# Kernel optimization log

Hardware: AMD Instinct MI355X
Metric: run time of the kernel (lower is better)

Reference implementation:

```python
import jax, jax.numpy as jnp
import numpy as np


def hadamard_matrix(n):
    # Recursive normalized Hadamard matrix of size 2^n (matches the torch code).
    H = np.array([[1.0]])
    for _ in range(n):
        H = np.block([[H, H], [H, -H]]) / np.sqrt(2.0)
    return jnp.asarray(H, dtype=jnp.float32)


def hadamard_conv(x, filt, bias, H):
    # x: (B, Cin, h, w); filt: (F, kh, kw); bias: (F, 1); H: (n, n)
    n = H.shape[0]
    F, kh, kw = filt.shape
    B, C = x.shape[0], x.shape[1]
    # zero-pad filters and data up to (n, n), then 2D Hadamard transform H A H
    kern = jnp.zeros((F, n, n), x.dtype).at[:, :kh, :kw].set(filt)
    kern_t = jnp.matmul(H, jnp.matmul(kern, H))            # (F, n, n)
    data = jnp.zeros((B, C, n, n), x.dtype).at[:, :, : x.shape[2], : x.shape[3]].set(x)
    data_t = jnp.matmul(H, jnp.matmul(data, H))            # (B, C, n, n)
    # Original: expand to (B, C, F, n, n), multiply by kern_t, inverse transform,
    # then sum over C. Since kern_t is independent of C and the transforms are
    # linear, sum over C first -- identical math, no huge intermediate.
    s = data_t.sum(axis=1)                                  # (B, n, n)
    prod = s[:, None, :, :] * kern_t[None, :, :, :]         # (B, F, n, n)
    out = jnp.matmul(H, jnp.matmul(prod, H))                # (B, F, n, n)
    return out + bias[:, 0][None, :, None, None]


def maxpool2(x):
    # 2x2 max pool, stride 2, on (B, C, H, W)
    return jax.lax.reduce_window(x, -jnp.inf, jax.lax.max, (1, 1, 2, 2), (1, 1, 2, 2), 'VALID')


def setup_inputs() -> dict:
    key = jax.random.key(0)
    ks = jax.random.split(key, 9)
    return {
        'x': jax.random.normal(ks[0], (2048, 3, 32, 32), dtype=jnp.float32),
        'filter1': jax.random.normal(ks[1], (32, 3, 3), dtype=jnp.float32),
        'bias1': jax.random.normal(ks[2], (32, 1), dtype=jnp.float32),
        'filter2': jax.random.normal(ks[3], (64, 3, 3), dtype=jnp.float32),
        'bias2': jax.random.normal(ks[4], (64, 1), dtype=jnp.float32),
        'fc1_w': jax.random.normal(ks[5], (512, 4096), dtype=jnp.float32) * 0.02,
        'fc1_b': jax.random.normal(ks[6], (512,), dtype=jnp.float32) * 0.02,
        'fc2_w': jax.random.normal(ks[7], (10, 512), dtype=jnp.float32) * 0.02,
        'fc2_b': jax.random.normal(ks[8], (10,), dtype=jnp.float32) * 0.02,
    }


def reference(x, filter1, bias1, filter2, bias2, fc1_w, fc1_b, fc2_w, fc2_b):
    H1 = hadamard_matrix(5)  # 32x32
    H2 = hadamard_matrix(4)  # 16x16
    out = hadamard_conv(x, filter1, bias1, H1)      # (B, 32, 32, 32)
    out = maxpool2(jax.nn.relu(out))                # (B, 32, 16, 16)
    out = hadamard_conv(out, filter2, bias2, H2)    # (B, 64, 16, 16)
    out = maxpool2(jax.nn.relu(out))                # (B, 64, 8, 8)
    out = out.reshape(-1, 4096)
    out = jax.nn.relu(out @ fc1_w.T + fc1_b)        # (B, 512)
    out = out @ fc2_w.T + fc2_b                     # (B, 10)
    return jax.nn.softmax(out, axis=1)
```

## Files before the change

### kernel.cpp

```cpp
#include <hip/hip_runtime.h>

#define DEVI __device__ __forceinline__

typedef __attribute__((ext_vector_type(8))) short short8x;
typedef __attribute__((ext_vector_type(4))) float float4x;

DEVI float shx(float v, int m) { return __shfl_xor(v, m, 64); }

DEVI unsigned bf16r(float v) {
  unsigned u = __float_as_uint(v);
  return (u + 0x7FFF + ((u >> 16) & 1)) >> 16;
}
DEVI void split2(float a, float b, unsigned& h, unsigned& l) {
  unsigned ra = bf16r(a), rb = bf16r(b);
  float fa = __uint_as_float(ra << 16), fb = __uint_as_float(rb << 16);
  unsigned la = bf16r(a - fa), lb = bf16r(b - fb);
  h = ra | (rb << 16);
  l = la | (lb << 16);
}

DEVI void gload16(const void* g, void* l) {
  __builtin_amdgcn_global_load_lds(
      (const __attribute__((address_space(1))) void*)g,
      (__attribute__((address_space(3))) void*)l, 16, 0, 0);
}

template <int MASK>
DEVI float lanex(float x) {
  if constexpr (MASK == 1)
    return __int_as_float(__builtin_amdgcn_update_dpp(
        0, __float_as_int(x), 0xB1, 0xF, 0xF, true));
  else if constexpr (MASK == 2)
    return __int_as_float(__builtin_amdgcn_update_dpp(
        0, __float_as_int(x), 0x4E, 0xF, 0xF, true));
  else
    return __int_as_float(__builtin_amdgcn_ds_swizzle(
        __float_as_int(x), (MASK << 10) | 0x1F));
}

__global__ __launch_bounds__(256) void k_conv(
    const float* __restrict__ x, const float* __restrict__ filt1,
    const float* __restrict__ bias1, const float* __restrict__ filt2,
    const float* __restrict__ bias2, unsigned short* __restrict__ Ah,
    unsigned short* __restrict__ Al) {
  __shared__ float sP[4 * 320];
  const int b = blockIdx.x;
  const int tid = threadIdx.x;
  const int wv = tid >> 6, t = tid & 63;

  float s0[16];
  {
    const float* xb = x + (size_t)b * 3072 + (t >> 1) * 32 + (t & 1) * 16;
#pragma unroll
    for (int q = 0; q < 4; ++q) {
      float4 a0 = *(const float4*)(xb + 4 * q);
      float4 a1 = *(const float4*)(xb + 1024 + 4 * q);
      float4 a2 = *(const float4*)(xb + 2048 + 4 * q);
      s0[4 * q + 0] = (a0.x + a1.x + a2.x) * (1.0f / 32.0f);
      s0[4 * q + 1] = (a0.y + a1.y + a2.y) * (1.0f / 32.0f);
      s0[4 * q + 2] = (a0.z + a1.z + a2.z) * (1.0f / 32.0f);
      s0[4 * q + 3] = (a0.w + a1.w + a2.w) * (1.0f / 32.0f);
    }
  }
  float s1[16], s2[16];
#pragma unroll
  for (int k = 0; k < 16; ++k) s1[k] = lanex<2>(s0[k]);
#pragma unroll
  for (int k = 0; k < 16; ++k) s2[k] = lanex<4>(s0[k]);

  float acc[8];
#pragma unroll
  for (int j = 0; j < 8; ++j) acc[j] = 0.0f;

  for (int i = 0; i < 8; ++i) {
    const int f = __builtin_amdgcn_readfirstlane(wv * 8 + i);
    const float* fp = filt1 + f * 9;
    float w[9];
#pragma unroll
    for (int k = 0; k < 9; ++k) w[k] = fp[k];
    const float bb = bias1[f];
    float c[8];
#pragma unroll
    for (int p = 0; p < 8; ++p) {
      const int ja = 2 * p, jb = ja ^ 1;
      const int ja2 = ja ^ 2, jb2 = jb ^ 2;
      float va = fmaf(w[0], s0[ja], bb);
      va = fmaf(w[1], s0[jb], va);
      va = fmaf(w[2], s0[ja2], va);
      va = fmaf(w[3], s1[ja], va);
      va = fmaf(w[4], s1[jb], va);
      va = fmaf(w[5], s1[ja2], va);
      va = fmaf(w[6], s2[ja], va);
      va = fmaf(w[7], s2[jb], va);
      va = fmaf(w[8], s2[ja2], va);
      float vb = fmaf(w[0], s0[jb], bb);
      vb = fmaf(w[1], s0[ja], vb);
      vb = fmaf(w[2], s0[jb2], vb);
      vb = fmaf(w[3], s1[jb], vb);
      vb = fmaf(w[4], s1[ja], vb);
      vb = fmaf(w[5], s1[jb2], vb);
      vb = fmaf(w[6], s2[jb], vb);
      vb = fmaf(w[7], s2[ja], vb);
      vb = fmaf(w[8], s2[jb2], vb);
      c[p] = fmaxf(fmaxf(va, vb), 0.0f);
    }
#pragma unroll
    for (int p = 0; p < 8; ++p) acc[p] += fmaxf(c[p], lanex<2>(c[p]));
  }

  if (!(t & 2)) {
    const int pb = wv * 320 + (t >> 2) * 20 + (t & 1) * 8;
    *(float4*)&sP[pb] = make_float4(acc[0], acc[1], acc[2], acc[3]);
    *(float4*)&sP[pb + 4] = make_float4(acc[4], acc[5], acc[6], acc[7]);
  }
  __syncthreads();

  const int f2s = t >> 4, rr = t & 15;
  float r0[16];
#pragma unroll
  for (int q = 0; q < 4; ++q) {
    float4 s = make_float4(0.f, 0.f, 0.f, 0.f);
#pragma unroll
    for (int w2 = 0; w2 < 4; ++w2) {
      const float4 v = *(const float4*)&sP[w2 * 320 + rr * 20 + 4 * q];
      s.x += v.x; s.y += v.y; s.z += v.z; s.w += v.w;
    }
    r0[4 * q + 0] = s.x * (1.0f / 16.0f);
    r0[4 * q + 1] = s.y * (1.0f / 16.0f);
    r0[4 * q + 2] = s.z * (1.0f / 16.0f);
    r0[4 * q + 3] = s.w * (1.0f / 16.0f);
  }
  float r1[16], r2[16];
#pragma unroll
  for (int k = 0; k < 16; ++k) r1[k] = lanex<1>(r0[k]);
#pragma unroll
  for (int k = 0; k < 16; ++k) r2[k] = lanex<2>(r0[k]);

#pragma unroll
  for (int it = 0; it < 4; ++it) {
    const int g = wv * 16 + it * 4 + f2s;
    const float* gp = filt2 + g * 9;
    float w[9];
#pragma unroll
    for (int k = 0; k < 9; ++k) w[k] = gp[k];
    const float bb = bias2[g];
    float c[8];
#pragma unroll
    for (int p = 0; p < 8; ++p) {
      const int ja = 2 * p, jb = ja ^ 1;
      const int ja2 = ja ^ 2, jb2 = jb ^ 2;
      float va = fmaf(w[0], r0[ja], bb);
      va = fmaf(w[1], r0[jb], va);
      va = fmaf(w[2], r0[ja2], va);
      va = fmaf(w[3], r1[ja], va);
      va = fmaf(w[4], r1[jb], va);
      va = fmaf(w[5], r1[ja2], va);
      va = fmaf(w[6], r2[ja], va);
      va = fmaf(w[7], r2[jb], va);
      va = fmaf(w[8], r2[ja2], va);
      float vb = fmaf(w[0], r0[jb], bb);
      vb = fmaf(w[1], r0[ja], vb);
      vb = fmaf(w[2], r0[jb2], vb);
      vb = fmaf(w[3], r1[jb], vb);
      vb = fmaf(w[4], r1[ja], vb);
      vb = fmaf(w[5], r1[jb2], vb);
      vb = fmaf(w[6], r2[jb], vb);
      vb = fmaf(w[7], r2[ja], vb);
      vb = fmaf(w[8], r2[jb2], vb);
      c[p] = fmaxf(fmaxf(va, vb), 0.0f);
    }
#pragma unroll
    for (int p = 0; p < 8; ++p) c[p] = fmaxf(c[p], lanex<1>(c[p]));
    if (!(t & 1)) {
      unsigned hh[4], ll[4];
#pragma unroll
      for (int j = 0; j < 4; ++j) split2(c[2 * j], c[2 * j + 1], hh[j], ll[j]);
      const size_t off = (size_t)b * 4096 + g * 64 + (rr >> 1) * 8;
      *(uint4*)(Ah + off) = make_uint4(hh[0], hh[1], hh[2], hh[3]);
      *(uint4*)(Al + off) = make_uint4(ll[0], ll[1], ll[2], ll[3]);
    }
  }
}

__global__ __launch_bounds__(256) void k_wsplit(
    const float* __restrict__ W, unsigned short* __restrict__ Wh,
    unsigned short* __restrict__ Wl) {
  const int i = (blockIdx.x * 256 + threadIdx.x) * 4;
  float4 v = *(const float4*)(W + i);
  unsigned h0, l0, h1, l1;
  split2(v.x, v.y, h0, l0);
  split2(v.z, v.w, h1, l1);
  *(uint2*)(Wh + i) = make_uint2(h0, h1);
  *(uint2*)(Wl + i) = make_uint2(l0, l1);
}

__global__ __launch_bounds__(256) void k_fc1(
    const unsigned short* __restrict__ Ah, const unsigned short* __restrict__ Al,
    const unsigned short* __restrict__ Wh, const unsigned short* __restrict__ Wl,
    float* __restrict__ P, int M) {
  __shared__ __align__(16) unsigned char lds[49152];
  const int bid = blockIdx.x;
  const int low3 = bid & 7, rest = bid >> 3;
  const int nt = rest & 7;
  const int c = ((rest >> 3) << 3) | low3;
  const int mt = c >> 2, kidx = c & 3;
  const int m0 = mt * 128, n0 = nt * 64, k0 = kidx * 1024;

  const int tid = threadIdx.x;
  const int wv = tid >> 6, lane = tid & 63;
  const int wm = (wv >> 1) * 64, wn = (wv & 1) * 32;
  const int lm = lane & 15, lq = lane >> 4;

  float4x acc[4][2];
#pragma unroll
  for (int i = 0; i < 4; ++i)
#pragma unroll
    for (int j = 0; j < 2; ++j) acc[i][j] = (float4x){0.f, 0.f, 0.f, 0.f};

  auto stage = [&](int st, int bb) {
    const int kcol = k0 + st * 32;
    const int rj = lane >> 3;
    const int pj = lane & 7;
#pragma unroll
    for (int it = 0; it < 4; ++it) {
      const int rb = wv * 32 + it * 8;
      const int r = rb + rj;
      const int l = pj ^ (r & 7);
      const unsigned short* src = (l < 4) ? Ah : Al;
      const size_t go = (size_t)(m0 + r) * 4096 + kcol + (l & 3) * 8;
      gload16(src + go, lds + bb + rb * 128);
    }
#pragma unroll
    for (int it = 0; it < 2; ++it) {
      const int rb = wv * 16 + it * 8;
      const int r = rb + rj;
      const int l = pj ^ (r & 7);
      const unsigned short* src = (l < 4) ? Wh : Wl;
      const size_t go = (size_t)(n0 + r) * 4096 + kcol + (l & 3) * 8;
      gload16(src + go, lds + bb + 16384 + rb * 128);
    }
  };

  stage(0, 0);
  __syncthreads();

  for (int st = 0; st < 32; ++st) {
    const int bb = (st & 1) * 24576;
    if (st < 31) stage(st + 1, bb ^ 24576);

    short8x a_h[4], a_l[4], b_h[2], b_l[2];
#pragma unroll
    for (int fm = 0; fm < 4; ++fm) {
      const int r = wm + fm * 16 + lm;
      const unsigned char* base = lds + bb + r * 128;
      a_h[fm] = *(const short8x*)(base + (lq ^ (r & 7)) * 16);
      a_l[fm] = *(const short8x*)(base + ((lq ^ 4) ^ (r & 7)) * 16);
    }
#pragma unroll
    for (int fn = 0; fn < 2; ++fn) {
      const int r = wn + fn * 16 + lm;
      const unsigned char* base = lds + bb + 16384 + r * 128;
      b_h[fn] = *(const short8x*)(base + (lq ^ (r & 7)) * 16);
      b_l[fn] = *(const short8x*)(base + ((lq ^ 4) ^ (r & 7)) * 16);
    }
#pragma unroll
    for (int fm = 0; fm < 4; ++fm)
#pragma unroll
      for (int fn = 0; fn < 2; ++fn) {
        acc[fm][fn] = __builtin_amdgcn_mfma_f32_16x16x32_bf16(
            a_h[fm], b_h[fn], acc[fm][fn], 0, 0, 0);
        acc[fm][fn] = __builtin_amdgcn_mfma_f32_16x16x32_bf16(
            a_h[fm], b_l[fn], acc[fm][fn], 0, 0, 0);
        acc[fm][fn] = __builtin_amdgcn_mfma_f32_16x16x32_bf16(
            a_l[fm], b_h[fn], acc[fm][fn], 0, 0, 0);
      }
    __syncthreads();
  }

  float* Pp = P + (size_t)kidx * ((size_t)M * 512);
#pragma unroll
  for (int fm = 0; fm < 4; ++fm)
#pragma unroll
    for (int fn = 0; fn < 2; ++fn)
#pragma unroll
      for (int i = 0; i < 4; ++i) {
        const int r = m0 + wm + fm * 16 + lq * 4 + i;
        const int cc = n0 + wn + fn * 16 + lm;
        Pp[(size_t)r * 512 + cc] = acc[fm][fn][i];
      }
}

__global__ __launch_bounds__(256) void k_fc2(
    const float* __restrict__ P, const float* __restrict__ bias1,
    const float* __restrict__ W, const float* __restrict__ bias2,
    float* __restrict__ out, int M) {
  const int wv = threadIdx.x >> 6, t = threadIdx.x & 63;
  const int b = blockIdx.x * 4 + wv;
  const size_t ks = (size_t)M * 512;
  const float* pr = P + (size_t)b * 512 + t * 8;
  float4 u0 = *(const float4*)pr;
  float4 u1 = *(const float4*)(pr + 4);
#pragma unroll
  for (int k = 1; k < 4; ++k) {
    const float4 v0 = *(const float4*)(pr + k * ks);
    const float4 v1 = *(const float4*)(pr + k * ks + 4);
    u0.x += v0.x; u0.y += v0.y; u0.z += v0.z; u0.w += v0.w;
    u1.x += v1.x; u1.y += v1.y; u1.z += v1.z; u1.w += v1.w;
  }
  const float4 bb0 = *(const float4*)(bias1 + t * 8);
  const float4 bb1 = *(const float4*)(bias1 + t * 8 + 4);
  float a[8];
  a[0] = fmaxf(u0.x + bb0.x, 0.0f);
  a[1] = fmaxf(u0.y + bb0.y, 0.0f);
  a[2] = fmaxf(u0.z + bb0.z, 0.0f);
  a[3] = fmaxf(u0.w + bb0.w, 0.0f);
  a[4] = fmaxf(u1.x + bb1.x, 0.0f);
  a[5] = fmaxf(u1.y + bb1.y, 0.0f);
  a[6] = fmaxf(u1.z + bb1.z, 0.0f);
  a[7] = fmaxf(u1.w + bb1.w, 0.0f);
  float z[10];
#pragma unroll
  for (int o = 0; o < 10; ++o) {
    const float* wr = W + o * 512 + t * 8;
    const float4 w0 = *(const float4*)wr;
    const float4 w1 = *(const float4*)(wr + 4);
    float s = a[0] * w0.x;
    s = fmaf(a[1], w0.y, s);
    s = fmaf(a[2], w0.z, s);
    s = fmaf(a[3], w0.w, s);
    s = fmaf(a[4], w1.x, s);
    s = fmaf(a[5], w1.y, s);
    s = fmaf(a[6], w1.z, s);
    s = fmaf(a[7], w1.w, s);
    z[o] = s;
  }
#pragma unroll
  for (int m = 1; m < 64; m <<= 1) {
#pragma unroll
    for (int o = 0; o < 10; ++o) z[o] += shx(z[o], m);
  }
#pragma unroll
  for (int o = 0; o < 10; ++o) z[o] += bias2[o];
  float mx = z[0];
#pragma unroll
  for (int o = 1; o < 10; ++o) mx = fmaxf(mx, z[o]);
  float e[10];
  float ssum = 0.0f;
#pragma unroll
  for (int o = 0; o < 10; ++o) {
    e[o] = expf(z[o] - mx);
    ssum += e[o];
  }
  const float inv = 1.0f / ssum;
  if (t == 0) {
    float* dst = out + (size_t)b * 10;
#pragma unroll
    for (int o = 0; o < 10; ++o) dst[o] = e[o] * inv;
  }
}

extern "C" void kernel_launch(void* const* d_in, const int* in_sizes, int n_in,
                              void* d_out, int out_size, void* d_ws,
                              size_t ws_size, hipStream_t stream) {
  const float* x = (const float*)d_in[0];
  const float* f1 = (const float*)d_in[1];
  const float* b1 = (const float*)d_in[2];
  const float* f2 = (const float*)d_in[3];
  const float* b2 = (const float*)d_in[4];
  const float* fc1w = (const float*)d_in[5];
  const float* fc1b = (const float*)d_in[6];
  const float* fc2w = (const float*)d_in[7];
  const float* fc2b = (const float*)d_in[8];
  float* out = (float*)d_out;
  const int B = in_sizes[0] / 3072;

  char* w = (char*)d_ws;
  unsigned short* Ah = (unsigned short*)w;
  unsigned short* Al = (unsigned short*)(w + (size_t)B * 8192);
  unsigned short* Wh = (unsigned short*)(w + (size_t)2 * B * 8192);
  unsigned short* Wl = (unsigned short*)(w + (size_t)2 * B * 8192 + 4194304);
  float* P = (float*)(w + (size_t)2 * B * 8192 + 8388608);

  hipLaunchKernelGGL(k_wsplit, dim3(2048), dim3(256), 0, stream, fc1w, Wh, Wl);
  hipLaunchKernelGGL(k_conv, dim3(B), dim3(256), 0, stream, x, f1, b1, f2, b2,
                     Ah, Al);
  hipLaunchKernelGGL(k_fc1, dim3((B / 128) * 32), dim3(256), 0, stream, Ah, Al,
                     Wh, Wl, P, B);
  hipLaunchKernelGGL(k_fc2, dim3(B / 4), dim3(256), 0, stream, P, fc1b, fc2w,
                     fc2b, out, B);
}
```

Baseline: 154.8 us.

## Fuse weight split into conv kernel and triple-buffer smaller fc1 tiles

Folds the fc1 weight bf16 hi/lo split into the conv kernel as extra blocks, removing one launch. The fc1 GEMM tile shrinks from 128x64 to 64x64, doubling the grid to 1024 blocks, and the block-index mapping is reordered. The fc1 K-loop moves from double to triple buffering with explicit vmcnt waits and raw s_barrier, so loads two stages ahead overlap compute. Smaller tiles raise occupancy and parallelism but lower per-block data reuse, and the fc1 blocks now read each weight tile twice as often. The hardcoded 1024-block grid assumes B=2048, and the fixed vmcnt counts assume each stage issues exactly four loads per thread.

After: 159.8 us. +3.2%, slower.

```diff
diff --git a/kernel.cpp b/kernel.cpp
--- a/kernel.cpp
+++ b/kernel.cpp
@@ -42,10 +42,27 @@
     const float* __restrict__ x, const float* __restrict__ filt1,
     const float* __restrict__ bias1, const float* __restrict__ filt2,
     const float* __restrict__ bias2, unsigned short* __restrict__ Ah,
-    unsigned short* __restrict__ Al) {
+    unsigned short* __restrict__ Al, const float* __restrict__ fc1w,
+    unsigned short* __restrict__ Wh, unsigned short* __restrict__ Wl, int B) {
   __shared__ float sP[4 * 320];
   const int b = blockIdx.x;
   const int tid = threadIdx.x;
+
+  if (b >= B) {
+    const int wb = b - B;
+#pragma unroll
+    for (int q = 0; q < 4; ++q) {
+      const int i = wb * 4096 + q * 1024 + tid * 4;
+      float4 v = *(const float4*)(fc1w + i);
+      unsigned h0, l0, h1, l1;
+      split2(v.x, v.y, h0, l0);
+      split2(v.z, v.w, h1, l1);
+      *(uint2*)(Wh + i) = make_uint2(h0, h1);
+      *(uint2*)(Wl + i) = make_uint2(l0, l1);
+    }
+    return;
+  }
+
   const int wv = tid >> 6, t = tid & 63;
 
   float s0[16];
@@ -182,48 +199,33 @@
   }
 }
 
-__global__ __launch_bounds__(256) void k_wsplit(
-    const float* __restrict__ W, unsigned short* __restrict__ Wh,
-    unsigned short* __restrict__ Wl) {
-  const int i = (blockIdx.x * 256 + threadIdx.x) * 4;
-  float4 v = *(const float4*)(W + i);
-  unsigned h0, l0, h1, l1;
-  split2(v.x, v.y, h0, l0);
-  split2(v.z, v.w, h1, l1);
-  *(uint2*)(Wh + i) = make_uint2(h0, h1);
-  *(uint2*)(Wl + i) = make_uint2(l0, l1);
-}
-
 __global__ __launch_bounds__(256) void k_fc1(
     const unsigned short* __restrict__ Ah, const unsigned short* __restrict__ Al,
     const unsigned short* __restrict__ Wh, const unsigned short* __restrict__ Wl,
     float* __restrict__ P, int M) {
   __shared__ __align__(16) unsigned char lds[49152];
   const int bid = blockIdx.x;
-  const int low3 = bid & 7, rest = bid >> 3;
-  const int nt = rest & 7;
-  const int c = ((rest >> 3) << 3) | low3;
+  const int c = bid & 127, nt = bid >> 7;
   const int mt = c >> 2, kidx = c & 3;
-  const int m0 = mt * 128, n0 = nt * 64, k0 = kidx * 1024;
+  const int m0 = mt * 64, n0 = nt * 64, k0 = kidx * 1024;
 
   const int tid = threadIdx.x;
   const int wv = tid >> 6, lane = tid & 63;
-  const int wm = (wv >> 1) * 64, wn = (wv & 1) * 32;
+  const int wm = (wv >> 1) * 32, wn = (wv & 1) * 32;
   const int lm = lane & 15, lq = lane >> 4;
-
-  float4x acc[4][2];
-#pragma unroll
-  for (int i = 0; i < 4; ++i)
+  const int rj = lane >> 3, pj = lane & 7;
+
+  float4x acc[2][2];
+#pragma unroll
+  for (int i = 0; i < 2; ++i)
 #pragma unroll
     for (int j = 0; j < 2; ++j) acc[i][j] = (float4x){0.f, 0.f, 0.f, 0.f};
 
   auto stage = [&](int st, int bb) {
     const int kcol = k0 + st * 32;
-    const int rj = lane >> 3;
-    const int pj = lane & 7;
-#pragma unroll
-    for (int it = 0; it < 4; ++it) {
-      const int rb = wv * 32 + it * 8;
+#pragma unroll
+    for (int it = 0; it < 2; ++it) {
+      const int rb = wv * 16 + it * 8;
       const int r = rb + rj;
       const int l = pj ^ (r & 7);
       const unsigned short* src = (l < 4) ? Ah : Al;
@@ -237,20 +239,27 @@
       const int l = pj ^ (r & 7);
       const unsigned short* src = (l < 4) ? Wh : Wl;
       const size_t go = (size_t)(n0 + r) * 4096 + kcol + (l & 3) * 8;
-      gload16(src + go, lds + bb + 16384 + rb * 128);
+      gload16(src + go, lds + bb + 8192 + rb * 128);
     }
   };
 
   stage(0, 0);
-  __syncthreads();
+  stage(1, 16384);
+  asm volatile("s_waitcnt vmcnt(4) lgkmcnt(0)" ::: "memory");
+  __builtin_amdgcn_sched_barrier(0);
+  __builtin_amdgcn_s_barrier();
+  __builtin_amdgcn_sched_barrier(0);
 
   for (int st = 0; st < 32; ++st) {
-    const int bb = (st & 1) * 24576;
-    if (st < 31) stage(st + 1, bb ^ 24576);
-
-    short8x a_h[4], a_l[4], b_h[2], b_l[2];
-#pragma unroll
-    for (int fm = 0; fm < 4; ++fm) {
+    const int bb = (st % 3) * 16384;
+    if (st < 30) {
+      stage(st + 2, ((st + 2) % 3) * 16384);
+      __builtin_amdgcn_sched_barrier(0);
+    }
+
+    short8x a_h[2], a_l[2], b_h[2], b_l[2];
+#pragma unroll
+    for (int fm = 0; fm < 2; ++fm) {
       const int r = wm + fm * 16 + lm;
       const unsigned char* base = lds + bb + r * 128;
       a_h[fm] = *(const short8x*)(base + (lq ^ (r & 7)) * 16);
@@ -259,12 +268,12 @@
 #pragma unroll
     for (int fn = 0; fn < 2; ++fn) {
       const int r = wn + fn * 16 + lm;
-      const unsigned char* base = lds + bb + 16384 + r * 128;
+      const unsigned char* base = lds + bb + 8192 + r * 128;
       b_h[fn] = *(const short8x*)(base + (lq ^ (r & 7)) * 16);
       b_l[fn] = *(const short8x*)(base + ((lq ^ 4) ^ (r & 7)) * 16);
     }
 #pragma unroll
-    for (int fm = 0; fm < 4; ++fm)
+    for (int fm = 0; fm < 2; ++fm)
 #pragma unroll
       for (int fn = 0; fn < 2; ++fn) {
         acc[fm][fn] = __builtin_amdgcn_mfma_f32_16x16x32_bf16(
@@ -274,12 +283,21 @@
         acc[fm][fn] = __builtin_amdgcn_mfma_f32_16x16x32_bf16(
             a_l[fm], b_h[fn], acc[fm][fn], 0, 0, 0);
       }
-    __syncthreads();
+
+    if (st < 31) {
+      if (st < 29)
+        asm volatile("s_waitcnt vmcnt(4) lgkmcnt(0)" ::: "memory");
+      else
+        asm volatile("s_waitcnt vmcnt(0) lgkmcnt(0)" ::: "memory");
+      __builtin_amdgcn_sched_barrier(0);
+      __builtin_amdgcn_s_barrier();
+      __builtin_amdgcn_sched_barrier(0);
+    }
   }
 
   float* Pp = P + (size_t)kidx * ((size_t)M * 512);
 #pragma unroll
-  for (int fm = 0; fm < 4; ++fm)
+  for (int fm = 0; fm < 2; ++fm)
 #pragma unroll
     for (int fn = 0; fn < 2; ++fn)
 #pragma unroll
@@ -381,11 +399,10 @@
   unsigned short* Wl = (unsigned short*)(w + (size_t)2 * B * 8192 + 4194304);
   float* P = (float*)(w + (size_t)2 * B * 8192 + 8388608);
 
-  hipLaunchKernelGGL(k_wsplit, dim3(2048), dim3(256), 0, stream, fc1w, Wh, Wl);
-  hipLaunchKernelGGL(k_conv, dim3(B), dim3(256), 0, stream, x, f1, b1, f2, b2,
-                     Ah, Al);
-  hipLaunchKernelGGL(k_fc1, dim3((B / 128) * 32), dim3(256), 0, stream, Ah, Al,
-                     Wh, Wl, P, B);
+  hipLaunchKernelGGL(k_conv, dim3(B + 512), dim3(256), 0, stream, x, f1, b1,
+                     f2, b2, Ah, Al, fc1w, Wh, Wl, B);
+  hipLaunchKernelGGL(k_fc1, dim3(1024), dim3(256), 0, stream, Ah, Al, Wh, Wl,
+                     P, B);
   hipLaunchKernelGGL(k_fc2, dim3(B / 4), dim3(256), 0, stream, P, fc1b, fc2w,
                      fc2b, out, B);
 }
```
